# Kernel tuning notes

Measured on AMD Instinct MI355X. Metric: run time of the kernel, lower is better.

Reference implementation:

```python
import jax, jax.numpy as jnp
import numpy as np

D = 100  # input_size


def _gru_scan(x, h0, wi, wh, bi, bh):
    # x: [B,T,Din], h0: [B,H], wi: [3H,Din], wh: [3H,H]  (PyTorch r,z,n gate order)
    xw = jnp.einsum('btd,gd->btg', x, wi) + bi  # [B,T,3H]
    def step(h, xt):
        gh = h @ wh.T + bh
        xr, xz, xn = jnp.split(xt, 3, axis=-1)
        hr, hz, hn = jnp.split(gh, 3, axis=-1)
        r = jax.nn.sigmoid(xr + hr)
        z = jax.nn.sigmoid(xz + hz)
        n = jnp.tanh(xn + r * hn)
        hn2 = (1 - z) * n + z * h
        return hn2, hn2
    _, ys = jax.lax.scan(step, h0, jnp.swapaxes(xw, 0, 1))
    return jnp.swapaxes(ys, 0, 1)  # [B,T,H]


def _bigru(x, wi, wh, bi, bh):
    B = x.shape[0]
    H = wh.shape[-1]
    h0 = jnp.zeros((B, H), x.dtype)
    f = _gru_scan(x, h0, wi[0], wh[0], bi[0], bh[0])
    b = _gru_scan(x[:, ::-1], h0, wi[1], wh[1], bi[1], bh[1])[:, ::-1]
    return jnp.concatenate([f, b], axis=-1)


def _gru_cell(x, h, wi, wh, bi, bh):
    gx = x @ wi.T + bi
    gh = h @ wh.T + bh
    xr, xz, xn = jnp.split(gx, 3, axis=-1)
    hr, hz, hn = jnp.split(gh, 3, axis=-1)
    r = jax.nn.sigmoid(xr + hr)
    z = jax.nn.sigmoid(xz + hz)
    n = jnp.tanh(xn + r * hn)
    return (1 - z) * n + z * h


def setup_inputs() -> dict:
    key = jax.random.key(0)
    ks = iter(jax.random.split(key, 40))
    def n(shape, s=0.08):
        return (jax.random.normal(next(ks), shape) * s).astype(jnp.float32)
    B, T, L, V = 32, 512, 64, 400000
    inp = {
        'x_word': jax.random.randint(next(ks), (B, T), 0, V),
        'x_query': jax.random.randint(next(ks), (B, L), 0, V),
        'embed': n((V, D), 0.3),
        'ctx_wi': n((2, 3 * D, D)), 'ctx_wh': n((2, 3 * D, D)),
        'ctx_bi': n((2, 3 * D)), 'ctx_bh': n((2, 3 * D)),
        'mod0_wi': n((2, 3 * D, 8 * D)), 'mod0_wh': n((2, 3 * D, D)),
        'mod0_bi': n((2, 3 * D)), 'mod0_bh': n((2, 3 * D)),
        'mod1_wi': n((2, 3 * D, 2 * D)), 'mod1_wh': n((2, 3 * D, D)),
        'mod1_bi': n((2, 3 * D)), 'mod1_bh': n((2, 3 * D)),
        'w_sim': n((6 * D,)),
        'enc_wi': n((12 * D, 2 * D)), 'enc_wh': n((12 * D, 4 * D)),
        'enc_bi': n((12 * D,)), 'enc_bh': n((12 * D,)),
        'dec_wi': n((12 * D, 2 * D)), 'dec_wh': n((12 * D, 4 * D)),
        'dec_bi': n((12 * D,)), 'dec_bh': n((12 * D,)),
        'w1': n((2 * D, 4 * D)), 'w2': n((2 * D, 4 * D)), 'vt': n((2 * D,)),
    }
    return inp


def reference(x_word, x_query, embed, ctx_wi, ctx_wh, ctx_bi, ctx_bh,
              mod0_wi, mod0_wh, mod0_bi, mod0_bh, mod1_wi, mod1_wh, mod1_bi, mod1_bh,
              w_sim, enc_wi, enc_wh, enc_bi, enc_bh, dec_wi, dec_wh, dec_bi, dec_bh,
              w1, w2, vt):
    B, T = x_word.shape
    # shared bidirectional context encoder over both context and query
    h = _bigru(embed[x_word], ctx_wi, ctx_wh, ctx_bi, ctx_bh)   # [B,T,2D]
    u = _bigru(embed[x_query], ctx_wi, ctx_wh, ctx_bi, ctx_bh)  # [B,L,2D]
    # trilinear similarity W @ cat(h,u,h*u), fused (no [B,T,L,6D] materialization)
    w1s, w2s, w3s = jnp.split(w_sim, 3)
    S = (jnp.einsum('btd,d->bt', h, w1s)[:, :, None]
         + jnp.einsum('bld,d->bl', u, w2s)[:, None, :]
         + jnp.einsum('btd,bld->btl', h * w3s, u))               # [B,T,L]
    c2q = jnp.einsum('btl,bld->btd', jax.nn.softmax(S, axis=-1), u)
    b_att = jax.nn.softmax(jnp.max(S, axis=2), axis=-1)          # [B,T]
    q2c = jnp.einsum('bt,btd->bd', b_att, h)[:, None, :]         # [B,1,2D]
    G = jnp.concatenate([h, c2q, h * c2q, h * q2c], axis=-1)     # [B,T,8D]
    # 2-layer bidirectional modeling GRU
    M = _bigru(G, mod0_wi, mod0_wh, mod0_bi, mod0_bh)
    M = _bigru(M, mod1_wi, mod1_wh, mod1_bi, mod1_bh)            # [B,T,2D]
    # pointer network
    enc = _gru_scan(M, jnp.zeros((B, 4 * D), M.dtype), enc_wi, enc_wh, enc_bi, enc_bh)  # [B,T,4D]
    enc_w1 = jnp.einsum('bth,ph->btp', enc, w1)                  # precompute W1 @ enc
    hid = jnp.zeros((B, 4 * D), M.dtype)
    dec_in = jnp.zeros((B, 2 * D), M.dtype)  # never updated (as in original)
    probs = []
    for _ in range(2):  # answers = 2 (start, end)
        hid = _gru_cell(dec_in, hid, dec_wi, dec_wh, dec_bi, dec_bh)
        blend = jnp.tanh(enc_w1 + (hid @ w2.T)[:, None, :])      # [B,T,2D]
        out = jnp.einsum('btp,p->bt', blend, vt)
        probs.append(jax.nn.log_softmax(out, axis=-1))
    return jnp.stack(probs, axis=1)  # [B,2,T]
```

## Files before the change

kernel.cpp:

```cpp
#include <hip/hip_runtime.h>
#include <hip/hip_bf16.h>

typedef __hip_bfloat16 bf16;
typedef unsigned long long u64;
typedef __attribute__((ext_vector_type(8))) short s8v;
typedef __attribute__((ext_vector_type(4))) short s4v;
typedef __attribute__((ext_vector_type(4))) float f4v;

#define DEV __device__ __forceinline__

DEV float to_f32(float x) { return x; }
DEV float to_f32(bf16 x) { return __bfloat162float(x); }
DEV void store_c(float* p, float v) { *p = v; }
DEV void store_c(bf16* p, float v) { *p = __float2bfloat16(v); }
DEV float sigmf(float x) { return 1.f / (1.f + __expf(-x)); }

__global__ void gather_embed_bf(const int* __restrict__ idx, const float* __restrict__ embed,
                                bf16* __restrict__ out, int ntok) {
  int i = blockIdx.x * blockDim.x + threadIdx.x;
  if (i >= ntok * 100) return;
  int t = i / 100;
  int d = i - t * 100;
  out[i] = __float2bfloat16(embed[(size_t)idx[t] * 100 + d]);
}

__global__ void cvt_all(const float* __restrict__ s0, bf16* __restrict__ d0,
                        const float* __restrict__ s1, bf16* __restrict__ d1,
                        const float* __restrict__ s2, bf16* __restrict__ d2,
                        const float* __restrict__ s3, bf16* __restrict__ d3,
                        const float* __restrict__ s4, bf16* __restrict__ d4) {
  int i = blockIdx.x * blockDim.x + threadIdx.x;
  if (i < 60000) d0[i] = __float2bfloat16(s0[i]);
  i -= 60000;
  if (i >= 0 && i < 480000) d1[i] = __float2bfloat16(s1[i]);
  i -= 480000;
  if (i >= 0 && i < 120000) d2[i] = __float2bfloat16(s2[i]);
  i -= 120000;
  if (i >= 0 && i < 240000) d3[i] = __float2bfloat16(s3[i]);
  i -= 240000;
  if (i >= 0 && i < 80000) d4[i] = __float2bfloat16(s4[i]);
}

template <typename TC, bool HAS_BIAS>
__global__ __launch_bounds__(256) void gemm_mfma(
    const bf16* __restrict__ A, const bf16* __restrict__ W,
    const float* __restrict__ bias, TC* __restrict__ C,
    int M, int N, int K) {
  __shared__ short Als[128 * 32];
  __shared__ short Wls[64 * 32];
  const int tid = threadIdx.x;
  const int m0 = blockIdx.x * 128;
  const int n0 = blockIdx.y * 64;
  const int lane = tid & 63;
  const int wv = tid >> 6;
  const int wm = wv >> 1, wn = wv & 1;
  const int lq = lane >> 4, lr = lane & 15;
  const int arow = tid >> 1;
  const int ah = tid & 1;
  const int wrow = (tid & 127) >> 1;

  f4v acc[4][2];
#pragma unroll
  for (int i = 0; i < 4; ++i)
#pragma unroll
    for (int j = 0; j < 2; ++j) acc[i][j] = (f4v){0.f, 0.f, 0.f, 0.f};

  for (int k0 = 0; k0 < K; k0 += 32) {
#pragma unroll
    for (int ss = 0; ss < 2; ++ss) {
      int s = 2 * ah + ss;
      int kk = k0 + s * 8;
      short* dst = &Als[arow * 32 + s * 8];
      const short* src = (const short*)(A + (size_t)(m0 + arow) * K + kk);
      if (kk + 8 <= K) {
        *(s4v*)dst = *(const s4v*)src;
        *(s4v*)(dst + 4) = *(const s4v*)(src + 4);
      } else {
#pragma unroll
        for (int j = 0; j < 8; ++j) dst[j] = (kk + j < K) ? src[j] : (short)0;
      }
    }
    if (tid < 128) {
      int nrow = n0 + wrow;
#pragma unroll
      for (int ss = 0; ss < 2; ++ss) {
        int s = 2 * (tid & 1) + ss;
        int kk = k0 + s * 8;
        short* dst = &Wls[wrow * 32 + s * 8];
        if (nrow < N) {
          const short* src = (const short*)(W + (size_t)nrow * K + kk);
          if (kk + 8 <= K) {
            *(s4v*)dst = *(const s4v*)src;
            *(s4v*)(dst + 4) = *(const s4v*)(src + 4);
          } else {
#pragma unroll
            for (int j = 0; j < 8; ++j) dst[j] = (kk + j < K) ? src[j] : (short)0;
          }
        } else {
#pragma unroll
          for (int j = 0; j < 8; ++j) dst[j] = (short)0;
        }
      }
    }
    __syncthreads();
    s8v af[4], bfr[2];
#pragma unroll
    for (int mi = 0; mi < 4; ++mi) {
      int r = wm * 64 + mi * 16 + lr;
      af[mi] = *(const s8v*)&Als[r * 32 + lq * 8];
    }
#pragma unroll
    for (int ni = 0; ni < 2; ++ni) {
      int r = wn * 32 + ni * 16 + lr;
      bfr[ni] = *(const s8v*)&Wls[r * 32 + lq * 8];
    }
#pragma unroll
    for (int mi = 0; mi < 4; ++mi)
#pragma unroll
      for (int ni = 0; ni < 2; ++ni)
        acc[mi][ni] = __builtin_amdgcn_mfma_f32_16x16x32_bf16(af[mi], bfr[ni], acc[mi][ni], 0, 0, 0);
    __syncthreads();
  }
#pragma unroll
  for (int mi = 0; mi < 4; ++mi) {
#pragma unroll
    for (int ni = 0; ni < 2; ++ni) {
      int n = n0 + wn * 32 + ni * 16 + lr;
      if (n >= N) continue;
      float bv = HAS_BIAS ? bias[n] : 0.f;
#pragma unroll
      for (int r = 0; r < 4; ++r) {
        int m = m0 + wm * 64 + mi * 16 + lq * 4 + r;
        store_c(&C[(size_t)m * N + n], acc[mi][ni][r] + bv);
      }
    }
  }
}

template <typename TO>
__global__ __launch_bounds__(320) void gru_scan100_reg(
    const bf16* __restrict__ xw,
    const float* __restrict__ wh,
    const float* __restrict__ bh,
    TO* __restrict__ out,
    int T) {
  const int b = blockIdx.x, dir = blockIdx.y;
  __shared__ float h_s[100];
  __shared__ float g_s[300];
  const int tid = threadIdx.x;
  float w[100];
  float bias = 0.f;
  if (tid < 300) {
    const float* wrow = wh + (size_t)dir * 30000 + (size_t)tid * 100;
#pragma unroll
    for (int c = 0; c < 25; ++c) {
      float4 v = *(const float4*)(wrow + 4 * c);
      w[4 * c] = v.x; w[4 * c + 1] = v.y; w[4 * c + 2] = v.z; w[4 * c + 3] = v.w;
    }
    bias = bh[dir * 300 + tid];
  }
  if (tid < 100) h_s[tid] = 0.f;
  float pxr = 0.f, pxz = 0.f, pxn = 0.f;
  if (tid < 100) {
    int t0 = dir ? (T - 1) : 0;
    size_t base = ((size_t)b * T + t0) * 600 + dir * 300;
    pxr = to_f32(xw[base + tid]);
    pxz = to_f32(xw[base + 100 + tid]);
    pxn = to_f32(xw[base + 200 + tid]);
  }
  __syncthreads();
  for (int step = 0; step < T; ++step) {
    int t = dir ? (T - 1 - step) : step;
    if (tid < 300) {
      float4 hbuf[25];
#pragma unroll
      for (int c = 0; c < 25; ++c) hbuf[c] = *(const float4*)(&h_s[4 * c]);
      float a0 = bias, a1 = 0.f, a2 = 0.f, a3 = 0.f;
#pragma unroll
      for (int c = 0; c < 25; ++c) {
        a0 += w[4 * c] * hbuf[c].x; a1 += w[4 * c + 1] * hbuf[c].y;
        a2 += w[4 * c + 2] * hbuf[c].z; a3 += w[4 * c + 3] * hbuf[c].w;
      }
      g_s[tid] = (a0 + a1) + (a2 + a3);
    }
    __syncthreads();
    if (tid < 100) {
      float rr = sigmf(pxr + g_s[tid]);
      float zz = sigmf(pxz + g_s[100 + tid]);
      float nn = tanhf(pxn + rr * g_s[200 + tid]);
      float hn = (1.f - zz) * nn + zz * h_s[tid];
      h_s[tid] = hn;
      store_c(&out[((size_t)b * T + t) * 200 + dir * 100 + tid], hn);
      if (step + 1 < T) {
        int tn = dir ? (T - 2 - step) : (step + 1);
        size_t basen = ((size_t)b * T + tn) * 600 + dir * 300;
        pxr = to_f32(xw[basen + tid]);
        pxz = to_f32(xw[basen + 100 + tid]);
        pxn = to_f32(xw[basen + 200 + tid]);
      }
    }
    __syncthreads();
  }
}

__global__ __launch_bounds__(640) void gru_scan_enc_tag(
    const bf16* __restrict__ xw,
    const float* __restrict__ wh,
    const float* __restrict__ bh,
    bf16* __restrict__ out,
    u64* __restrict__ hx,
    int T) {
  const int b = blockIdx.x, s = blockIdx.y;
  __shared__ float h_s[400];
  __shared__ float g_s[150];
  const int tid = threadIdx.x;
  const int g = tid >> 2, p = tid & 3;
  const bool active = (tid < 600);
  float w[100];
  float bias = 0.f;
  if (active) {
    int i = g % 50, grp = g / 50;
    int gidx = grp * 400 + s * 50 + i;
    const float* wrow = wh + (size_t)gidx * 400 + p * 100;
#pragma unroll
    for (int c = 0; c < 25; ++c) {
      float4 v = *(const float4*)(wrow + 4 * c);
      w[4 * c] = v.x; w[4 * c + 1] = v.y; w[4 * c + 2] = v.z; w[4 * c + 3] = v.w;
    }
    if (p == 0) bias = bh[gidx];
  }
  for (int k = tid; k < 400; k += 640) h_s[k] = 0.f;
  const int myi = s * 50 + tid;
  float pxr = 0.f, pxz = 0.f, pxn = 0.f;
  if (tid < 50) {
    size_t base0 = (size_t)b * T * 1200;
    pxr = to_f32(xw[base0 + myi]);
    pxz = to_f32(xw[base0 + 400 + myi]);
    pxn = to_f32(xw[base0 + 800 + myi]);
  }
  __syncthreads();

  for (int t = 0; t < T; ++t) {
    if (active) {
      const int hb = p * 100;
      float4 hbuf[25];
#pragma unroll
      for (int c = 0; c < 25; ++c) hbuf[c] = *(const float4*)(&h_s[hb + 4 * c]);
      float a0 = bias, a1 = 0.f, a2 = 0.f, a3 = 0.f;
#pragma unroll
      for (int c = 0; c < 25; ++c) {
        a0 += w[4 * c] * hbuf[c].x; a1 += w[4 * c + 1] * hbuf[c].y;
        a2 += w[4 * c + 2] * hbuf[c].z; a3 += w[4 * c + 3] * hbuf[c].w;
      }
      float acc = (a0 + a1) + (a2 + a3);
      acc += __shfl_xor(acc, 1);
      acc += __shfl_xor(acc, 2);
      if (p == 0) g_s[g] = acc;
    }
    __syncthreads();
    const int par = (t + 1) & 1;
    u64* hxp = hx + ((size_t)b * 2 + par) * 400;
    if (tid < 50) {
      float rr = sigmf(pxr + g_s[tid]);
      float zz = sigmf(pxz + g_s[50 + tid]);
      float nn = tanhf(pxn + rr * g_s[100 + tid]);
      float hn = (1.f - zz) * nn + zz * h_s[myi];
      out[((size_t)b * T + t) * 400 + myi] = __float2bfloat16(hn);
      h_s[myi] = hn;
      u64 pack = (u64)__float_as_uint(hn) | ((u64)(unsigned)(t + 1) << 32);
      __hip_atomic_store(&hxp[myi], pack, __ATOMIC_RELAXED, __HIP_MEMORY_SCOPE_AGENT);
      if (t + 1 < T) {
        size_t basen = ((size_t)b * T + (t + 1)) * 1200;
        pxr = to_f32(xw[basen + myi]);
        pxz = to_f32(xw[basen + 400 + myi]);
        pxn = to_f32(xw[basen + 800 + myi]);
      }
    }
    if (tid < 400 && (tid / 50) != s) {
      const u64* src = &hxp[tid];
      u64 v;
      for (;;) {
        v = __hip_atomic_load(src, __ATOMIC_RELAXED, __HIP_MEMORY_SCOPE_AGENT);
        if ((unsigned)(v >> 32) == (unsigned)(t + 1)) break;
        __builtin_amdgcn_s_sleep(1);
      }
      h_s[tid] = __uint_as_float((unsigned)v);
    }
    __syncthreads();
  }
}

__global__ __launch_bounds__(256) void attn_main(
    const float* __restrict__ h,
    const float* __restrict__ u,
    const float* __restrict__ w_sim,
    float* __restrict__ c2q,
    float* __restrict__ smax,
    int T) {
  const int b = blockIdx.x;
  const int t0 = blockIdx.y * 32;
  __shared__ float u_s[64 * 201];
  __shared__ float w1_s[200], w2_s[200], w3_s[200];
  __shared__ float th_s[32], tu_s[64];
  __shared__ float hw3_s[200];
  __shared__ float Sp[4][64];
  __shared__ float A_s[64];
  const int tid = threadIdx.x;
  for (int i = tid; i < 64 * 200; i += 256) {
    int l = i / 200, d = i - l * 200;
    u_s[l * 201 + d] = u[((size_t)b * 64 + l) * 200 + d];
  }
  if (tid < 200) {
    w1_s[tid] = w_sim[tid];
    w2_s[tid] = w_sim[200 + tid];
    w3_s[tid] = w_sim[400 + tid];
  }
  __syncthreads();
  {
    int r = tid >> 2, sg = tid & 3;
    float p = 0.f;
    for (int j = 0; j < 50; ++j) p += u_s[r * 201 + sg * 50 + j] * w2_s[sg * 50 + j];
    p += __shfl_down(p, 2);
    p += __shfl_down(p, 1);
    if (sg == 0) tu_s[r] = p;
  }
  {
    int r = tid >> 3, sg = tid & 7;
    float p = 0.f;
    const float* hr = h + ((size_t)b * T + t0 + r) * 200 + sg * 25;
    for (int j = 0; j < 25; ++j) p += hr[j] * w1_s[sg * 25 + j];
    p += __shfl_down(p, 4);
    p += __shfl_down(p, 2);
    p += __shfl_down(p, 1);
    if (sg == 0) th_s[r] = p;
  }
  __syncthreads();
  for (int tt = 0; tt < 32; ++tt) {
    int t = t0 + tt;
    if (tid < 200) hw3_s[tid] = h[((size_t)b * T + t) * 200 + tid] * w3_s[tid];
    __syncthreads();
    int l = tid & 63, q = tid >> 6;
    float p = 0.f;
    for (int d = q * 50; d < q * 50 + 50; ++d) p += hw3_s[d] * u_s[l * 201 + d];
    Sp[q][l] = p;
    __syncthreads();
    if (tid < 64) {
      float s = th_s[tt] + tu_s[l] + Sp[0][l] + Sp[1][l] + Sp[2][l] + Sp[3][l];
      float m = s;
      for (int off = 32; off; off >>= 1) m = fmaxf(m, __shfl_xor(m, off));
      float e = __expf(s - m);
      float ssum = e;
      for (int off = 32; off; off >>= 1) ssum += __shfl_xor(ssum, off);
      A_s[l] = e / ssum;
      if (l == 0) smax[b * T + t] = m;
    }
    __syncthreads();
    if (tid < 200) {
      float acc = 0.f;
      for (int l2 = 0; l2 < 64; ++l2) acc += A_s[l2] * u_s[l2 * 201 + tid];
      c2q[((size_t)b * T + t) * 200 + tid] = acc;
    }
    __syncthreads();
  }
}

__global__ __launch_bounds__(256) void softmax_q2c(
    const float* __restrict__ smaxv, const float* __restrict__ h,
    float* __restrict__ q2c, int T) {
  int b = blockIdx.x;
  int tid = threadIdx.x;
  __shared__ float red[256];
  __shared__ float batt_s[512];
  float m = -1e30f;
  for (int t = tid; t < T; t += 256) m = fmaxf(m, smaxv[b * T + t]);
  red[tid] = m;
  __syncthreads();
  for (int s = 128; s; s >>= 1) {
    if (tid < s) red[tid] = fmaxf(red[tid], red[tid + s]);
    __syncthreads();
  }
  m = red[0];
  __syncthreads();
  float sum = 0.f;
  for (int t = tid; t < T; t += 256) {
    float e = __expf(smaxv[b * T + t] - m);
    batt_s[t] = e;
    sum += e;
  }
  red[tid] = sum;
  __syncthreads();
  for (int s = 128; s; s >>= 1) {
    if (tid < s) red[tid] += red[tid + s];
    __syncthreads();
  }
  float inv = 1.f / red[0];
  __syncthreads();
  if (tid < 200) {
    float acc = 0.f;
    for (int t = 0; t < T; ++t) acc += batt_s[t] * h[((size_t)b * T + t) * 200 + tid];
    q2c[b * 200 + tid] = acc * inv;
  }
}

__global__ void build_G(const float* __restrict__ h, const float* __restrict__ c2q,
                        const float* __restrict__ q2c, bf16* __restrict__ G, int T) {
  size_t i = (size_t)blockIdx.x * blockDim.x + threadIdx.x;
  if (i >= (size_t)32 * T * 200) return;
  size_t row = i / 200;
  int d = (int)(i - row * 200);
  int b = (int)(row / T);
  float hv = h[i];
  float cv = c2q[i];
  float qv = q2c[b * 200 + d];
  bf16* g = G + row * 800;
  g[d] = __float2bfloat16(hv);
  g[200 + d] = __float2bfloat16(cv);
  g[400 + d] = __float2bfloat16(hv * cv);
  g[600 + d] = __float2bfloat16(hv * qv);
}

__global__ __launch_bounds__(512) void decoder_small(
    const float* __restrict__ dwh, const float* __restrict__ dbi,
    const float* __restrict__ dbh, const float* __restrict__ w2,
    float* __restrict__ d2out) {
  __shared__ float hid[400];
  __shared__ float hid2[400];
  __shared__ float gh[1200];
  const int tid = threadIdx.x;
  if (tid < 400) {
    float r = sigmf(dbi[tid] + dbh[tid]);
    float z = sigmf(dbi[400 + tid] + dbh[400 + tid]);
    float n = tanhf(dbi[800 + tid] + r * dbh[800 + tid]);
    hid[tid] = (1.f - z) * n;
  }
  __syncthreads();
  if (tid < 200) {
    float a = 0.f;
    for (int k = 0; k < 400; ++k) a += w2[(size_t)tid * 400 + k] * hid[k];
    d2out[tid] = a;
  }
  for (int j = tid; j < 1200; j += 512) {
    float a = dbh[j];
    for (int k = 0; k < 400; ++k) a += dwh[(size_t)j * 400 + k] * hid[k];
    gh[j] = a;
  }
  __syncthreads();
  if (tid < 400) {
    float r = sigmf(dbi[tid] + gh[tid]);
    float z = sigmf(dbi[400 + tid] + gh[400 + tid]);
    float n = tanhf(dbi[800 + tid] + r * gh[800 + tid]);
    hid2[tid] = (1.f - z) * n + z * hid[tid];
  }
  __syncthreads();
  if (tid < 200) {
    float a = 0.f;
    for (int k = 0; k < 400; ++k) a += w2[(size_t)tid * 400 + k] * hid2[k];
    d2out[200 + tid] = a;
  }
}

__global__ __launch_bounds__(64) void logits_kernel(
    const float* __restrict__ encw1, const float* __restrict__ d2,
    const float* __restrict__ vt, float* __restrict__ outp, int T) {
  int row = blockIdx.x;
  int b = row / T, t = row - b * T;
  int lane = threadIdx.x;
  const float* e = encw1 + (size_t)row * 200;
  float s0 = 0.f, s1 = 0.f;
  for (int p = lane; p < 200; p += 64) {
    float ev = e[p], v = vt[p];
    s0 += tanhf(ev + d2[p]) * v;
    s1 += tanhf(ev + d2[200 + p]) * v;
  }
  for (int off = 32; off; off >>= 1) {
    s0 += __shfl_down(s0, off);
    s1 += __shfl_down(s1, off);
  }
  if (lane == 0) {
    outp[((size_t)b * 2 + 0) * T + t] = s0;
    outp[((size_t)b * 2 + 1) * T + t] = s1;
  }
}

__global__ __launch_bounds__(256) void log_softmax_T(float* __restrict__ x, int T) {
  int row = blockIdx.x;
  float* p = x + (size_t)row * T;
  __shared__ float red[256];
  int tid = threadIdx.x;
  float m = -1e30f;
  for (int t = tid; t < T; t += 256) m = fmaxf(m, p[t]);
  red[tid] = m;
  __syncthreads();
  for (int s = 128; s; s >>= 1) {
    if (tid < s) red[tid] = fmaxf(red[tid], red[tid + s]);
    __syncthreads();
  }
  m = red[0];
  __syncthreads();
  float sum = 0.f;
  for (int t = tid; t < T; t += 256) sum += __expf(p[t] - m);
  red[tid] = sum;
  __syncthreads();
  for (int s = 128; s; s >>= 1) {
    if (tid < s) red[tid] += red[tid + s];
    __syncthreads();
  }
  float lse = m + __logf(red[0]);
  __syncthreads();
  for (int t = tid; t < T; t += 256) p[t] = p[t] - lse;
}

extern "C" void kernel_launch(void* const* d_in, const int* in_sizes, int n_in,
                              void* d_out, int out_size, void* d_ws, size_t ws_size,
                              hipStream_t stream) {
  (void)in_sizes; (void)n_in; (void)out_size; (void)ws_size;
  const int B = 32, T = 512, L = 64;
  const int BT = B * T;
  const int BL = B * L;

  const int* x_word = (const int*)d_in[0];
  const int* x_query = (const int*)d_in[1];
  const float* embed = (const float*)d_in[2];
  const float* ctx_wi = (const float*)d_in[3];
  const float* ctx_wh = (const float*)d_in[4];
  const float* ctx_bi = (const float*)d_in[5];
  const float* ctx_bh = (const float*)d_in[6];
  const float* mod0_wi = (const float*)d_in[7];
  const float* mod0_wh = (const float*)d_in[8];
  const float* mod0_bi = (const float*)d_in[9];
  const float* mod0_bh = (const float*)d_in[10];
  const float* mod1_wi = (const float*)d_in[11];
  const float* mod1_wh = (const float*)d_in[12];
  const float* mod1_bi = (const float*)d_in[13];
  const float* mod1_bh = (const float*)d_in[14];
  const float* w_sim = (const float*)d_in[15];
  const float* enc_wi = (const float*)d_in[16];
  const float* enc_wh = (const float*)d_in[17];
  const float* enc_bi = (const float*)d_in[18];
  const float* enc_bh = (const float*)d_in[19];
  const float* dec_wh = (const float*)d_in[21];
  const float* dec_bi = (const float*)d_in[22];
  const float* dec_bh = (const float*)d_in[23];
  const float* w1 = (const float*)d_in[24];
  const float* w2 = (const float*)d_in[25];
  const float* vt = (const float*)d_in[26];
  float* out_f = (float*)d_out;

  char* ws = (char*)d_ws;
  size_t off = 0;
  auto alloc = [&](size_t bytes) -> void* {
    void* p = ws + off;
    off += (bytes + 255) & ~(size_t)255;
    return p;
  };
  u64* hx = (u64*)alloc((size_t)B * 2 * 400 * 8);
  bf16* ewbf = (bf16*)alloc((size_t)BT * 100 * 2);
  bf16* eqbf = (bf16*)alloc((size_t)BL * 100 * 2);
  bf16* ctx_wibf = (bf16*)alloc((size_t)60000 * 2);
  bf16* mod0_wibf = (bf16*)alloc((size_t)480000 * 2);
  bf16* mod1_wibf = (bf16*)alloc((size_t)120000 * 2);
  bf16* enc_wibf = (bf16*)alloc((size_t)240000 * 2);
  bf16* w1bf = (bf16*)alloc((size_t)80000 * 2);
  char* RA = (char*)alloc((size_t)BT * 1200 * 2);
  bf16* xwFB = (bf16*)RA;
  bf16* xwe = (bf16*)RA;
  bf16* xwq = (bf16*)alloc((size_t)BL * 600 * 2);
  char* RB = (char*)alloc((size_t)BT * 800 * 2);
  bf16* G = (bf16*)RB;
  bf16* enc_outbf = (bf16*)RB;
  char* RC = (char*)alloc((size_t)2 * BT * 200 * 4);
  float* h_cat = (float*)RC;
  float* c2q = (float*)(RC + (size_t)BT * 200 * 4);
  bf16* M0bf = (bf16*)c2q;
  bf16* Mxbf = (bf16*)h_cat;
  float* encw1 = c2q;
  float* u_cat = (float*)alloc((size_t)BL * 200 * 4);
  float* smaxb = (float*)alloc((size_t)BT * 4);
  float* q2cb = (float*)alloc((size_t)B * 200 * 4);
  float* d2 = (float*)alloc((size_t)400 * 4);

  hipMemsetAsync(hx, 0, (size_t)B * 2 * 400 * 8, stream);

  cvt_all<<<(980000 + 255) / 256, 256, 0, stream>>>(ctx_wi, ctx_wibf, mod0_wi, mod0_wibf,
                                                    mod1_wi, mod1_wibf, enc_wi, enc_wibf,
                                                    w1, w1bf);
  gather_embed_bf<<<(BT * 100 + 255) / 256, 256, 0, stream>>>(x_word, embed, ewbf, BT);
  gather_embed_bf<<<(BL * 100 + 255) / 256, 256, 0, stream>>>(x_query, embed, eqbf, BL);

  gemm_mfma<bf16, true><<<dim3(BT / 128, 10), 256, 0, stream>>>(ewbf, ctx_wibf, ctx_bi, xwFB, BT, 600, 100);
  gemm_mfma<bf16, true><<<dim3(BL / 128, 10), 256, 0, stream>>>(eqbf, ctx_wibf, ctx_bi, xwq, BL, 600, 100);

  gru_scan100_reg<float><<<dim3(B, 2), 320, 0, stream>>>(xwFB, ctx_wh, ctx_bh, h_cat, T);
  gru_scan100_reg<float><<<dim3(B, 2), 320, 0, stream>>>(xwq, ctx_wh, ctx_bh, u_cat, L);

  attn_main<<<dim3(B, T / 32), 256, 0, stream>>>(h_cat, u_cat, w_sim, c2q, smaxb, T);
  softmax_q2c<<<B, 256, 0, stream>>>(smaxb, h_cat, q2cb, T);
  build_G<<<(BT * 200 + 255) / 256, 256, 0, stream>>>(h_cat, c2q, q2cb, G, T);

  gemm_mfma<bf16, true><<<dim3(BT / 128, 10), 256, 0, stream>>>(G, mod0_wibf, mod0_bi, xwFB, BT, 600, 800);
  gru_scan100_reg<bf16><<<dim3(B, 2), 320, 0, stream>>>(xwFB, mod0_wh, mod0_bh, M0bf, T);

  gemm_mfma<bf16, true><<<dim3(BT / 128, 10), 256, 0, stream>>>(M0bf, mod1_wibf, mod1_bi, xwFB, BT, 600, 200);
  gru_scan100_reg<bf16><<<dim3(B, 2), 320, 0, stream>>>(xwFB, mod1_wh, mod1_bh, Mxbf, T);

  gemm_mfma<bf16, true><<<dim3(BT / 128, (1200 + 63) / 64), 256, 0, stream>>>(Mxbf, enc_wibf, enc_bi, xwe, BT, 1200, 200);
  gru_scan_enc_tag<<<dim3(B, 8), 640, 0, stream>>>(xwe, enc_wh, enc_bh, enc_outbf, hx, T);
  gemm_mfma<float, false><<<dim3(BT / 128, (200 + 63) / 64), 256, 0, stream>>>(enc_outbf, w1bf, nullptr, encw1, BT, 200, 400);

  decoder_small<<<1, 512, 0, stream>>>(dec_wh, dec_bi, dec_bh, w2, d2);
  logits_kernel<<<BT, 64, 0, stream>>>(encw1, d2, vt, out_f, T);
  log_softmax_T<<<B * 2, 256, 0, stream>>>(out_f, T);
}
```

Before: 3.340 ms.

## Fuse embedding gather into GEMM, merge context scans, fuse logits with log-softmax

The embedding gather and bf16 conversion now happen inside the first GEMM's A-tile load, so the intermediate bf16 embedding buffers and two gather kernels go away. The context and query GRU scans run in one launch with a doubled grid, so the short query scan overlaps the long context scan instead of running after it. The logits and log-softmax kernels are fused into one block per batch row. The fused softmax hardcodes T=512 through its 512-thread block and shared arrays, and there are fewer blocks in the logits stage.

```diff
diff --git a/kernel.cpp b/kernel.cpp
--- a/kernel.cpp
+++ b/kernel.cpp
@@ -14,15 +14,7 @@
 DEV void store_c(float* p, float v) { *p = v; }
 DEV void store_c(bf16* p, float v) { *p = __float2bfloat16(v); }
 DEV float sigmf(float x) { return 1.f / (1.f + __expf(-x)); }
-
-__global__ void gather_embed_bf(const int* __restrict__ idx, const float* __restrict__ embed,
-                                bf16* __restrict__ out, int ntok) {
-  int i = blockIdx.x * blockDim.x + threadIdx.x;
-  if (i >= ntok * 100) return;
-  int t = i / 100;
-  int d = i - t * 100;
-  out[i] = __float2bfloat16(embed[(size_t)idx[t] * 100 + d]);
-}
+DEV short f2bs(float x) { bf16 h = __float2bfloat16(x); return *(short*)&h; }
 
 __global__ void cvt_all(const float* __restrict__ s0, bf16* __restrict__ d0,
                         const float* __restrict__ s1, bf16* __restrict__ d1,
@@ -41,9 +33,10 @@
   if (i >= 0 && i < 80000) d4[i] = __float2bfloat16(s4[i]);
 }
 
-template <typename TC, bool HAS_BIAS>
+template <typename TC, bool HAS_BIAS, bool GATHER>
 __global__ __launch_bounds__(256) void gemm_mfma(
-    const bf16* __restrict__ A, const bf16* __restrict__ W,
+    const bf16* __restrict__ A, const int* __restrict__ idx,
+    const float* __restrict__ embedp, const bf16* __restrict__ W,
     const float* __restrict__ bias, TC* __restrict__ C,
     int M, int N, int K) {
   __shared__ short Als[128 * 32];
@@ -59,6 +52,9 @@
   const int ah = tid & 1;
   const int wrow = (tid & 127) >> 1;
 
+  int vrow = 0;
+  if (GATHER) vrow = idx[m0 + arow];
+
   f4v acc[4][2];
 #pragma unroll
   for (int i = 0; i < 4; ++i)
@@ -71,13 +67,28 @@
       int s = 2 * ah + ss;
       int kk = k0 + s * 8;
       short* dst = &Als[arow * 32 + s * 8];
-      const short* src = (const short*)(A + (size_t)(m0 + arow) * K + kk);
-      if (kk + 8 <= K) {
-        *(s4v*)dst = *(const s4v*)src;
-        *(s4v*)(dst + 4) = *(const s4v*)(src + 4);
+      if (GATHER) {
+        const float* src = embedp + (size_t)vrow * 100 + kk;
+        if (kk + 8 <= K) {
+          float4 a4 = *(const float4*)src;
+          float4 b4 = *(const float4*)(src + 4);
+          s4v lo = {f2bs(a4.x), f2bs(a4.y), f2bs(a4.z), f2bs(a4.w)};
+          s4v hi = {f2bs(b4.x), f2bs(b4.y), f2bs(b4.z), f2bs(b4.w)};
+          *(s4v*)dst = lo;
+          *(s4v*)(dst + 4) = hi;
+        } else {
+#pragma unroll
+          for (int j = 0; j < 8; ++j) dst[j] = (kk + j < K) ? f2bs(src[j]) : (short)0;
+        }
       } else {
-#pragma unroll
-        for (int j = 0; j < 8; ++j) dst[j] = (kk + j < K) ? src[j] : (short)0;
+        const short* src = (const short*)(A + (size_t)(m0 + arow) * K + kk);
+        if (kk + 8 <= K) {
+          *(s4v*)dst = *(const s4v*)src;
+          *(s4v*)(dst + 4) = *(const s4v*)(src + 4);
+        } else {
+#pragma unroll
+          for (int j = 0; j < 8; ++j) dst[j] = (kk + j < K) ? src[j] : (short)0;
+        }
       }
     }
     if (tid < 128) {
@@ -138,13 +149,18 @@
 }
 
 template <typename TO>
-__global__ __launch_bounds__(320) void gru_scan100_reg(
-    const bf16* __restrict__ xw,
+__global__ __launch_bounds__(320) void gru_scan100_dual(
+    const bf16* __restrict__ xw0, const bf16* __restrict__ xw1,
     const float* __restrict__ wh,
     const float* __restrict__ bh,
-    TO* __restrict__ out,
-    int T) {
-  const int b = blockIdx.x, dir = blockIdx.y;
+    TO* __restrict__ out0, TO* __restrict__ out1,
+    int T0, int T1) {
+  const int b = blockIdx.x;
+  const int y = blockIdx.y;
+  const int which = y >> 1, dir = y & 1;
+  const bf16* xw = which ? xw1 : xw0;
+  TO* out = which ? out1 : out0;
+  const int T = which ? T1 : T0;
   __shared__ float h_s[100];
   __shared__ float g_s[300];
   const int tid = threadIdx.x;
@@ -291,12 +307,9 @@
 }
 
 __global__ __launch_bounds__(256) void attn_main(
-    const float* __restrict__ h,
-    const float* __restrict__ u,
-    const float* __restrict__ w_sim,
-    float* __restrict__ c2q,
-    float* __restrict__ smax,
-    int T) {
+    const float* __restrict__ h, const float* __restrict__ u,
+    const float* __restrict__ w_sim, float* __restrict__ c2q,
+    float* __restrict__ smax, int T) {
   const int b = blockIdx.x;
   const int t0 = blockIdx.y * 32;
   __shared__ float u_s[64 * 201];
@@ -459,55 +472,48 @@
   }
 }
 
-__global__ __launch_bounds__(64) void logits_kernel(
+__global__ __launch_bounds__(512) void logits_lsm(
     const float* __restrict__ encw1, const float* __restrict__ d2,
     const float* __restrict__ vt, float* __restrict__ outp, int T) {
-  int row = blockIdx.x;
-  int b = row / T, t = row - b * T;
-  int lane = threadIdx.x;
-  const float* e = encw1 + (size_t)row * 200;
-  float s0 = 0.f, s1 = 0.f;
-  for (int p = lane; p < 200; p += 64) {
-    float ev = e[p], v = vt[p];
-    s0 += tanhf(ev + d2[p]) * v;
-    s1 += tanhf(ev + d2[200 + p]) * v;
-  }
-  for (int off = 32; off; off >>= 1) {
-    s0 += __shfl_down(s0, off);
-    s1 += __shfl_down(s1, off);
-  }
-  if (lane == 0) {
-    outp[((size_t)b * 2 + 0) * T + t] = s0;
-    outp[((size_t)b * 2 + 1) * T + t] = s1;
-  }
-}
-
-__global__ __launch_bounds__(256) void log_softmax_T(float* __restrict__ x, int T) {
-  int row = blockIdx.x;
-  float* p = x + (size_t)row * T;
-  __shared__ float red[256];
-  int tid = threadIdx.x;
-  float m = -1e30f;
-  for (int t = tid; t < T; t += 256) m = fmaxf(m, p[t]);
-  red[tid] = m;
-  __syncthreads();
-  for (int s = 128; s; s >>= 1) {
-    if (tid < s) red[tid] = fmaxf(red[tid], red[tid + s]);
-    __syncthreads();
-  }
-  m = red[0];
-  __syncthreads();
-  float sum = 0.f;
-  for (int t = tid; t < T; t += 256) sum += __expf(p[t] - m);
-  red[tid] = sum;
-  __syncthreads();
-  for (int s = 128; s; s >>= 1) {
-    if (tid < s) red[tid] += red[tid + s];
-    __syncthreads();
-  }
-  float lse = m + __logf(red[0]);
-  __syncthreads();
-  for (int t = tid; t < T; t += 256) p[t] = p[t] - lse;
+  int b = blockIdx.x;
+  __shared__ float lg[2][512];
+  __shared__ float red[512];
+  const int tid = threadIdx.x;
+  const int wave = tid >> 6, lane = tid & 63;
+  for (int r = wave; r < T; r += 8) {
+    const float* e = encw1 + ((size_t)b * T + r) * 200;
+    float s0 = 0.f, s1 = 0.f;
+    for (int p = lane; p < 200; p += 64) {
+      float ev = e[p], v = vt[p];
+      s0 += tanhf(ev + d2[p]) * v;
+      s1 += tanhf(ev + d2[200 + p]) * v;
+    }
+    for (int off = 32; off; off >>= 1) {
+      s0 += __shfl_down(s0, off);
+      s1 += __shfl_down(s1, off);
+    }
+    if (lane == 0) { lg[0][r] = s0; lg[1][r] = s1; }
+  }
+  __syncthreads();
+  for (int it = 0; it < 2; ++it) {
+    red[tid] = lg[it][tid];
+    __syncthreads();
+    for (int s = 256; s; s >>= 1) {
+      if (tid < s) red[tid] = fmaxf(red[tid], red[tid + s]);
+      __syncthreads();
+    }
+    float m = red[0];
+    __syncthreads();
+    red[tid] = __expf(lg[it][tid] - m);
+    __syncthreads();
+    for (int s = 256; s; s >>= 1) {
+      if (tid < s) red[tid] += red[tid + s];
+      __syncthreads();
+    }
+    float lse = m + __logf(red[0]);
+    __syncthreads();
+    outp[((size_t)b * 2 + it) * T + tid] = lg[it][tid] - lse;
+  }
 }
 
 extern "C" void kernel_launch(void* const* d_in, const int* in_sizes, int n_in,
@@ -554,8 +560,6 @@
     return p;
   };
   u64* hx = (u64*)alloc((size_t)B * 2 * 400 * 8);
-  bf16* ewbf = (bf16*)alloc((size_t)BT * 100 * 2);
-  bf16* eqbf = (bf16*)alloc((size_t)BL * 100 * 2);
   bf16* ctx_wibf = (bf16*)alloc((size_t)60000 * 2);
   bf16* mod0_wibf = (bf16*)alloc((size_t)480000 * 2);
   bf16* mod1_wibf = (bf16*)alloc((size_t)120000 * 2);
@@ -584,30 +588,35 @@
   cvt_all<<<(980000 + 255) / 256, 256, 0, stream>>>(ctx_wi, ctx_wibf, mod0_wi, mod0_wibf,
                                                     mod1_wi, mod1_wibf, enc_wi, enc_wibf,
                                                     w1, w1bf);
-  gather_embed_bf<<<(BT * 100 + 255) / 256, 256, 0, stream>>>(x_word, embed, ewbf, BT);
-  gather_embed_bf<<<(BL * 100 + 255) / 256, 256, 0, stream>>>(x_query, embed, eqbf, BL);
-
-  gemm_mfma<bf16, true><<<dim3(BT / 128, 10), 256, 0, stream>>>(ewbf, ctx_wibf, ctx_bi, xwFB, BT, 600, 100);
-  gemm_mfma<bf16, true><<<dim3(BL / 128, 10), 256, 0, stream>>>(eqbf, ctx_wibf, ctx_bi, xwq, BL, 600, 100);
-
-  gru_scan100_reg<float><<<dim3(B, 2), 320, 0, stream>>>(xwFB, ctx_wh, ctx_bh, h_cat, T);
-  gru_scan100_reg<float><<<dim3(B, 2), 320, 0, stream>>>(xwq, ctx_wh, ctx_bh, u_cat, L);
+
+  gemm_mfma<bf16, true, true><<<dim3(BT / 128, 10), 256, 0, stream>>>(
+      nullptr, x_word, embed, ctx_wibf, ctx_bi, xwFB, BT, 600, 100);
+  gemm_mfma<bf16, true, true><<<dim3(BL / 128, 10), 256, 0, stream>>>(
+      nullptr, x_query, embed, ctx_wibf, ctx_bi, xwq, BL, 600, 100);
+
+  gru_scan100_dual<float><<<dim3(B, 4), 320, 0, stream>>>(
+      xwFB, xwq, ctx_wh, ctx_bh, h_cat, u_cat, T, L);
 
   attn_main<<<dim3(B, T / 32), 256, 0, stream>>>(h_cat, u_cat, w_sim, c2q, smaxb, T);
   softmax_q2c<<<B, 256, 0, stream>>>(smaxb, h_cat, q2cb, T);
   build_G<<<(BT * 200 + 255) / 256, 256, 0, stream>>>(h_cat, c2q, q2cb, G, T);
 
-  gemm_mfma<bf16, true><<<dim3(BT / 128, 10), 256, 0, stream>>>(G, mod0_wibf, mod0_bi, xwFB, BT, 600, 800);
-  gru_scan100_reg<bf16><<<dim3(B, 2), 320, 0, stream>>>(xwFB, mod0_wh, mod0_bh, M0bf, T);
-
-  gemm_mfma<bf16, true><<<dim3(BT / 128, 10), 256, 0, stream>>>(M0bf, mod1_wibf, mod1_bi, xwFB, BT, 600, 200);
-  gru_scan100_reg<bf16><<<dim3(B, 2), 320, 0, stream>>>(xwFB, mod1_wh, mod1_bh, Mxbf, T);
-
-  gemm_mfma<bf16, true><<<dim3(BT / 128, (1200 + 63) / 64), 256, 0, stream>>>(Mxbf, enc_wibf, enc_bi, xwe, BT, 1200, 200);
+  gemm_mfma<bf16, true, false><<<dim3(BT / 128, 10), 256, 0, stream>>>(
+      G, nullptr, nullptr, mod0_wibf, mod0_bi, xwFB, BT, 600, 800);
+  gru_scan100_dual<bf16><<<dim3(B, 2), 320, 0, stream>>>(
+      xwFB, nullptr, mod0_wh, mod0_bh, M0bf, nullptr, T, T);
+
+  gemm_mfma<bf16, true, false><<<dim3(BT / 128, 10), 256, 0, stream>>>(
+      M0bf, nullptr, nullptr, mod1_wibf, mod1_bi, xwFB, BT, 600, 200);
+  gru_scan100_dual<bf16><<<dim3(B, 2), 320, 0, stream>>>(
+      xwFB, nullptr, mod1_wh, mod1_bh, Mxbf, nullptr, T, T);
+
+  gemm_mfma<bf16, true, false><<<dim3(BT / 128, (1200 + 63) / 64), 256, 0, stream>>>(
+      Mxbf, nullptr, nullptr, enc_wibf, enc_bi, xwe, BT, 1200, 200);
   gru_scan_enc_tag<<<dim3(B, 8), 640, 0, stream>>>(xwe, enc_wh, enc_bh, enc_outbf, hx, T);
-  gemm_mfma<float, false><<<dim3(BT / 128, (200 + 63) / 64), 256, 0, stream>>>(enc_outbf, w1bf, nullptr, encw1, BT, 200, 400);
+  gemm_mfma<float, false, false><<<dim3(BT / 128, (200 + 63) / 64), 256, 0, stream>>>(
+      enc_outbf, nullptr, nullptr, w1bf, nullptr, encw1, BT, 200, 400);
 
   decoder_small<<<1, 512, 0, stream>>>(dec_wh, dec_bi, dec_bh, w2, d2);
-  logits_kernel<<<BT, 64, 0, stream>>>(encw1, d2, vt, out_f, T);
-  log_softmax_T<<<B * 2, 256, 0, stream>>>(out_f, T);
-}
+  logits_lsm<<<B, 512, 0, stream>>>(encw1, d2, vt, out_f, T);
+}
```

After: 3.396 ms. About the same (+1.7%).
